# Kernel tuning notes

Measured on AMD Instinct MI355X. Metric: run time of the kernel, lower is better.

## Reference

```python
import jax, jax.numpy as jnp
import numpy as np

N_NODES = 100000


def sage_conv(x, edge_index, W_l, b_l, W_r):
    # PyG SAGEConv (mean aggr): out = lin_l(mean_j x_j) + lin_r(x_i)
    src = edge_index[0]
    dst = edge_index[1]
    msg_sum = jax.ops.segment_sum(x[src], dst, num_segments=N_NODES)  # [N, d]
    deg = jax.ops.segment_sum(jnp.ones(src.shape[0], dtype=x.dtype), dst,
                              num_segments=N_NODES)  # [N]
    mean = msg_sum / jnp.maximum(deg, 1.0)[:, None]
    return mean @ W_l + b_l + x @ W_r


def setup_inputs() -> dict:
    key = jax.random.key(0)
    ks = jax.random.split(key, 8)
    d_in, hidden, d_out = 128, 256, 128
    n_edges = 1600000
    x = jax.random.normal(ks[0], (N_NODES, d_in), dtype=jnp.float32)
    edge_index = jax.random.randint(ks[1], (2, n_edges), 0, N_NODES, dtype=jnp.int64)
    s1 = 1.0 / np.sqrt(d_in)
    s2 = 1.0 / np.sqrt(hidden)
    return {
        "x": x,
        "edge_index": edge_index,
        "W_l1": jax.random.uniform(ks[2], (d_in, hidden), jnp.float32, -s1, s1),
        "b_l1": jnp.zeros((hidden,), jnp.float32),
        "W_r1": jax.random.uniform(ks[3], (d_in, hidden), jnp.float32, -s1, s1),
        "W_l2": jax.random.uniform(ks[4], (hidden, d_out), jnp.float32, -s2, s2),
        "b_l2": jnp.zeros((d_out,), jnp.float32),
        "W_r2": jax.random.uniform(ks[5], (hidden, d_out), jnp.float32, -s2, s2),
    }


def reference(x, edge_index, W_l1, b_l1, W_r1, W_l2, b_l2, W_r2):
    h = jax.nn.relu(sage_conv(x, edge_index, W_l1, b_l1, W_r1))
    return sage_conv(h, edge_index, W_l2, b_l2, W_r2)
```

## Files before the change

kernel.cpp:

```cpp
#include <hip/hip_runtime.h>

#define N_NODES 100000
#define NPAD 100096
#define NBLK 391

using bf16x8 = __attribute__((ext_vector_type(8))) short;
using f32x4  = __attribute__((ext_vector_type(4))) float;

__device__ inline short f2bf(float f) {
    unsigned int u = __float_as_uint(f);
    unsigned int r = (u + 0x7FFFu + ((u >> 16) & 1u)) >> 16;
    return (short)r;
}
__device__ inline float bf2f_lo(unsigned int w) { return __uint_as_float(w << 16); }
__device__ inline float bf2f_hi(unsigned int w) { return __uint_as_float(w & 0xFFFF0000u); }

__device__ inline bool xcd_map(int bid, int& row, int& col) {
    const int RP = (NBLK + 7) / 8;
    const int xcd = bid & 7;
    const int i = bid >> 3;
    row = xcd * RP + (i >> 1);
    col = i & 1;
    return row < NBLK;
}
#define GEMM_GRID (8 * 2 * ((NBLK + 7) / 8))

__global__ __launch_bounds__(256)
void cbuck_kernel(const int* __restrict__ dst, int* __restrict__ bucket_cnt, int E) {
    __shared__ int cnt[NBLK];
    const int tid = threadIdx.x;
    for (int i = tid; i < NBLK; i += 256) cnt[i] = 0;
    __syncthreads();
    const int e0 = blockIdx.x * 4096;
    #pragma unroll
    for (int k = 0; k < 16; ++k) {
        int e = e0 + k * 256 + tid;
        if (e < E) atomicAdd(&cnt[dst[e] >> 8], 1);
    }
    __syncthreads();
    for (int i = tid; i < NBLK; i += 256)
        if (cnt[i]) atomicAdd(&bucket_cnt[i], cnt[i]);
}

__global__ void scan391_kernel(const int* __restrict__ bucket_cnt, int* __restrict__ bucket_base,
                               int* __restrict__ bucket_cursor, int* __restrict__ offsets) {
    __shared__ int s[512];
    int t = threadIdx.x;
    int v = (t < NBLK) ? bucket_cnt[t] : 0;
    s[t] = v;
    __syncthreads();
    #pragma unroll
    for (int off = 1; off < 512; off <<= 1) {
        int u = (t >= off) ? s[t - off] : 0;
        __syncthreads();
        s[t] += u;
        __syncthreads();
    }
    if (t < NBLK) {
        int excl = s[t] - v;
        bucket_base[t] = excl;
        bucket_cursor[t] = excl;
    }
    if (t == NBLK - 1) {
        bucket_base[NBLK] = s[t];
        offsets[N_NODES] = s[t];
    }
}

__global__ __launch_bounds__(256)
void bin_kernel(const int* __restrict__ src, const int* __restrict__ dst,
                int* __restrict__ bucket_cursor, unsigned int* __restrict__ bin, int E) {
    __shared__ int cnt[NBLK];
    __shared__ int base_l[NBLK];
    const int tid = threadIdx.x;
    const int e0 = blockIdx.x * 4096;
    for (int i = tid; i < NBLK; i += 256) cnt[i] = 0;
    __syncthreads();
    int myb[16]; unsigned myv[16];
    #pragma unroll
    for (int k = 0; k < 16; ++k) {
        int e = e0 + k * 256 + tid;
        if (e < E) {
            int d = dst[e];
            myb[k] = d >> 8;
            myv[k] = (unsigned)src[e] | ((unsigned)(d & 255) << 20);
            atomicAdd(&cnt[myb[k]], 1);
        } else myb[k] = -1;
    }
    __syncthreads();
    for (int i = tid; i < NBLK; i += 256) {
        int c = cnt[i];
        base_l[i] = c ? atomicAdd(&bucket_cursor[i], c) : 0;
        cnt[i] = 0;
    }
    __syncthreads();
    #pragma unroll
    for (int k = 0; k < 16; ++k) {
        if (myb[k] >= 0) {
            int slot = base_l[myb[k]] + atomicAdd(&cnt[myb[k]], 1);
            bin[slot] = myv[k];
        }
    }
}

__global__ __launch_bounds__(256)
void place_kernel(const unsigned int* __restrict__ bin, const int* __restrict__ bucket_base,
                  int* __restrict__ offsets, int* __restrict__ sorted) {
    __shared__ int cnt[256];
    __shared__ int cur[256];
    __shared__ int wsum[4];
    const int b = blockIdx.x, tid = threadIdx.x;
    const int lane = tid & 63, wave = tid >> 6;
    const int s = bucket_base[b];
    const int e = bucket_base[b + 1];
    cnt[tid] = 0;
    __syncthreads();
    for (int i = s + tid; i < e; i += 256) atomicAdd(&cnt[bin[i] >> 20], 1);
    __syncthreads();
    int v = cnt[tid];
    int x = v;
    #pragma unroll
    for (int off = 1; off < 64; off <<= 1) {
        int t = __shfl_up(x, off, 64);
        if (lane >= off) x += t;
    }
    if (lane == 63) wsum[wave] = x;
    __syncthreads();
    int woff = 0;
    #pragma unroll
    for (int w = 0; w < 4; ++w) if (w < wave) woff += wsum[w];
    int excl = s + woff + x - v;
    cur[tid] = excl;
    int node = b * 256 + tid;
    if (node < N_NODES) offsets[node] = excl;
    __syncthreads();
    for (int i = s + tid; i < e; i += 256) {
        unsigned w = bin[i];
        int p = atomicAdd(&cur[w >> 20], 1);
        sorted[p] = (int)(w & 0xFFFFFu);
    }
}

__global__ __launch_bounds__(256)
void prep_kernel(const float* __restrict__ x, short* __restrict__ xrow, short* __restrict__ xpack,
                 const float* __restrict__ Wl1, const float* __restrict__ Wr1,
                 const float* __restrict__ Wl2, const float* __restrict__ Wr2,
                 short* __restrict__ wl1p, short* __restrict__ wr1p,
                 short* __restrict__ wl2p, short* __restrict__ wr2p) {
    int t = blockIdx.x * 256 + threadIdx.x;
    if (t < N_NODES * 16) {
        int row = t >> 4;
        int kc = (t & 15) << 3;
        const float4 v0 = *(const float4*)(x + (size_t)row * 128 + kc);
        const float4 v1 = *(const float4*)(x + (size_t)row * 128 + kc + 4);
        __align__(16) short s[8] = {f2bf(v0.x), f2bf(v0.y), f2bf(v0.z), f2bf(v0.w),
                                    f2bf(v1.x), f2bf(v1.y), f2bf(v1.z), f2bf(v1.w)};
        *(int4*)(xrow + (size_t)row * 128 + kc) = *(const int4*)s;
        size_t pidx = ((size_t)(row >> 4) * 16 + (kc >> 3)) * 128 + (size_t)(row & 15) * 8;
        *(int4*)(xpack + pidx) = *(const int4*)s;
        return;
    }
    int u = t - N_NODES * 16;
    if (u >= 4 * 32768) return;
    const int w = u >> 15;
    const int t2 = u & 32767;
    const float* W; short* P; int K, NC;
    if (w == 0)      { W = Wl1; P = wl1p; K = 128; NC = 256; }
    else if (w == 1) { W = Wr1; P = wr1p; K = 128; NC = 256; }
    else if (w == 2) { W = Wl2; P = wl2p; K = 256; NC = 128; }
    else             { W = Wr2; P = wr2p; K = 256; NC = 128; }
    int k = t2 / NC, c = t2 % NC;
    P[((size_t)(c >> 4) * (K >> 3) + (k >> 3)) * 128 + (size_t)(c & 15) * 8 + (k & 7)] = f2bf(W[t2]);
}

template<int MODE>
__global__ __launch_bounds__(512)
void aggregate128_kernel(const short* __restrict__ feat, const int* __restrict__ offsets,
                         const int* __restrict__ srcs,
                         short* __restrict__ outpack, float* __restrict__ outf) {
    int node = blockIdx.x * 8 + (threadIdx.x >> 6);
    if (node >= N_NODES) return;
    const int lane = threadIdx.x & 63;
    const int g = lane >> 4, p = lane & 15;
    const int s = offsets[node], e = offsets[node + 1];
    const float inv = 1.0f / (float)max(e - s, 1);
    float acc[8] = {0.f, 0.f, 0.f, 0.f, 0.f, 0.f, 0.f, 0.f};
    for (int j = s + g; j < e; j += 8) {
        const int j2 = j + 4;
        const bool h2 = (j2 < e);
        const int i0 = srcs[j];
        const int i1 = h2 ? srcs[j2] : i0;
        const uint4 w0 = *(const uint4*)(feat + (size_t)i0 * 128 + p * 8);
        const uint4 w1 = *(const uint4*)(feat + (size_t)i1 * 128 + p * 8);
        acc[0] += bf2f_lo(w0.x); acc[1] += bf2f_hi(w0.x);
        acc[2] += bf2f_lo(w0.y); acc[3] += bf2f_hi(w0.y);
        acc[4] += bf2f_lo(w0.z); acc[5] += bf2f_hi(w0.z);
        acc[6] += bf2f_lo(w0.w); acc[7] += bf2f_hi(w0.w);
        if (h2) {
            acc[0] += bf2f_lo(w1.x); acc[1] += bf2f_hi(w1.x);
            acc[2] += bf2f_lo(w1.y); acc[3] += bf2f_hi(w1.y);
            acc[4] += bf2f_lo(w1.z); acc[5] += bf2f_hi(w1.z);
            acc[6] += bf2f_lo(w1.w); acc[7] += bf2f_hi(w1.w);
        }
    }
    #pragma unroll
    for (int t = 0; t < 8; ++t) acc[t] += __shfl_xor(acc[t], 16, 64);
    #pragma unroll
    for (int t = 0; t < 8; ++t) acc[t] += __shfl_xor(acc[t], 32, 64);
    if (g != 0) return;
    if (MODE == 0) {
        __align__(16) short r[8];
        #pragma unroll
        for (int t = 0; t < 8; ++t) r[t] = f2bf(acc[t] * inv);
        size_t pidx = ((size_t)(node >> 4) * 16 + p) * 128 + (size_t)(node & 15) * 8;
        *(int4*)(outpack + pidx) = *(const int4*)r;
    } else {
        float* o = outf + (size_t)node * 128 + p * 8;
        float4 q0 = *(const float4*)o;
        float4 q1 = *(const float4*)(o + 4);
        q0.x += acc[0] * inv; q0.y += acc[1] * inv; q0.z += acc[2] * inv; q0.w += acc[3] * inv;
        q1.x += acc[4] * inv; q1.y += acc[5] * inv; q1.z += acc[6] * inv; q1.w += acc[7] * inv;
        *(float4*)o = q0;
        *(float4*)(o + 4) = q1;
    }
}

__global__ __launch_bounds__(256)
void gemm1_kernel(const short* __restrict__ A0, const short* __restrict__ A1,
                  const short* __restrict__ B0, const short* __restrict__ B1,
                  const float* __restrict__ bias, short* __restrict__ opack) {
    constexpr int KB = 16, KS = 4, S = 8;
    __shared__ float sC[4][32][132];
    int rowBlk, colHalf;
    if (!xcd_map(blockIdx.x, rowBlk, colHalf)) return;
    const int tid = threadIdx.x, wave = tid >> 6, lane = tid & 63;
    const int lhi = lane >> 4, llo = lane & 15;
    const int rowBase = rowBlk * 256 + wave * 64;
    const int colBase = colHalf * 128;
    const int rowTile = rowBase >> 4, colTile = colBase >> 4;

    f32x4 acc[4][8];
    #pragma unroll
    for (int i = 0; i < 4; ++i)
        #pragma unroll
        for (int j = 0; j < 8; ++j)
            #pragma unroll
            for (int r = 0; r < 4; ++r) acc[i][j][r] = 0.f;

    bf16x8 a[4];
    #pragma unroll
    for (int i = 0; i < 4; ++i)
        a[i] = *(const bf16x8*)(A0 + ((size_t)(rowTile + i) * KB + lhi) * 128 + (size_t)llo * 8);

    #pragma unroll
    for (int s = 0; s < S; ++s) {
        const short* B = (s >= KS) ? B1 : B0;
        const int kb = (s - (s >= KS ? KS : 0)) * 4 + lhi;
        bf16x8 b[8];
        #pragma unroll
        for (int j = 0; j < 8; ++j)
            b[j] = *(const bf16x8*)(B + ((size_t)(colTile + j) * KB + kb) * 128 + (size_t)llo * 8);
        bf16x8 an[4];
        if (s + 1 < S) {
            const int s1 = s + 1;
            const short* A = (s1 >= KS) ? A1 : A0;
            const int kb1 = (s1 - (s1 >= KS ? KS : 0)) * 4 + lhi;
            #pragma unroll
            for (int i = 0; i < 4; ++i)
                an[i] = *(const bf16x8*)(A + ((size_t)(rowTile + i) * KB + kb1) * 128 + (size_t)llo * 8);
        }
        #pragma unroll
        for (int i = 0; i < 4; ++i)
            #pragma unroll
            for (int j = 0; j < 8; ++j)
                acc[i][j] = __builtin_amdgcn_mfma_f32_16x16x32_bf16(a[i], b[j], acc[i][j], 0, 0, 0);
        if (s + 1 < S) {
            #pragma unroll
            for (int i = 0; i < 4; ++i) a[i] = an[i];
        }
    }

    #pragma unroll
    for (int j = 0; j < 8; ++j) {
        float bv = bias[colBase + j * 16 + llo];
        #pragma unroll
        for (int i = 0; i < 4; ++i)
            #pragma unroll
            for (int r = 0; r < 4; ++r)
                acc[i][j][r] = fmaxf(acc[i][j][r] + bv, 0.f);
    }

    #pragma unroll
    for (int half = 0; half < 2; ++half) {
        #pragma unroll
        for (int i2 = 0; i2 < 2; ++i2) {
            const int i = half * 2 + i2;
            #pragma unroll
            for (int j = 0; j < 8; ++j)
                #pragma unroll
                for (int r = 0; r < 4; ++r)
                    sC[wave][i2 * 16 + lhi * 4 + r][j * 16 + llo] = acc[i][j][r];
        }
        #pragma unroll
        for (int it = 0; it < 8; ++it) {
            const int r = it * 4 + (lane >> 4);
            const int c = (lane & 15) * 8;
            const int grow = rowBase + half * 32 + r;
            if (grow < N_NODES) {
                float4 v0 = *(const float4*)&sC[wave][r][c];
                float4 v1 = *(const float4*)&sC[wave][r][c + 4];
                __align__(16) short sv[8] = {f2bf(v0.x), f2bf(v0.y), f2bf(v0.z), f2bf(v0.w),
                                             f2bf(v1.x), f2bf(v1.y), f2bf(v1.z), f2bf(v1.w)};
                size_t pidx = ((size_t)(grow >> 4) * 32 + ((colBase + c) >> 3)) * 128
                            + (size_t)(grow & 15) * 8;
                *(int4*)(opack + pidx) = *(const int4*)sv;
            }
        }
    }
}

__global__ __launch_bounds__(256)
void gemm2_kernel(const short* __restrict__ A, const short* __restrict__ B0,
                  const short* __restrict__ B1, const float* __restrict__ bias,
                  short* __restrict__ prow, float* __restrict__ qf32) {
    constexpr int KB = 32, S = 8;
    __shared__ float sC[4][32][68];
    int rowBlk, colHalf;
    if (!xcd_map(blockIdx.x, rowBlk, colHalf)) return;
    const int tid = threadIdx.x, wave = tid >> 6, lane = tid & 63;
    const int lhi = lane >> 4, llo = lane & 15;
    const int rowBase = rowBlk * 256 + wave * 64;
    const int colBase = colHalf * 64;
    const int rowTile = rowBase >> 4, colTile = colBase >> 4;

    f32x4 accp[4][4], accq[4][4];
    #pragma unroll
    for (int i = 0; i < 4; ++i)
        #pragma unroll
        for (int j = 0; j < 4; ++j)
            #pragma unroll
            for (int r = 0; r < 4; ++r) { accp[i][j][r] = 0.f; accq[i][j][r] = 0.f; }

    bf16x8 a[4];
    #pragma unroll
    for (int i = 0; i < 4; ++i)
        a[i] = *(const bf16x8*)(A + ((size_t)(rowTile + i) * KB + lhi) * 128 + (size_t)llo * 8);

    #pragma unroll
    for (int s = 0; s < S; ++s) {
        const int kb = s * 4 + lhi;
        bf16x8 b0[4], b1[4];
        #pragma unroll
        for (int j = 0; j < 4; ++j) {
            b0[j] = *(const bf16x8*)(B0 + ((size_t)(colTile + j) * KB + kb) * 128 + (size_t)llo * 8);
            b1[j] = *(const bf16x8*)(B1 + ((size_t)(colTile + j) * KB + kb) * 128 + (size_t)llo * 8);
        }
        bf16x8 an[4];
        if (s + 1 < S) {
            const int kb1 = (s + 1) * 4 + lhi;
            #pragma unroll
            for (int i = 0; i < 4; ++i)
                an[i] = *(const bf16x8*)(A + ((size_t)(rowTile + i) * KB + kb1) * 128 + (size_t)llo * 8);
        }
        #pragma unroll
        for (int i = 0; i < 4; ++i)
            #pragma unroll
            for (int j = 0; j < 4; ++j) {
                accp[i][j] = __builtin_amdgcn_mfma_f32_16x16x32_bf16(a[i], b0[j], accp[i][j], 0, 0, 0);
                accq[i][j] = __builtin_amdgcn_mfma_f32_16x16x32_bf16(a[i], b1[j], accq[i][j], 0, 0, 0);
            }
        if (s + 1 < S) {
            #pragma unroll
            for (int i = 0; i < 4; ++i) a[i] = an[i];
        }
    }

    #pragma unroll
    for (int half = 0; half < 2; ++half) {
        #pragma unroll
        for (int i2 = 0; i2 < 2; ++i2) {
            const int i = half * 2 + i2;
            #pragma unroll
            for (int j = 0; j < 4; ++j)
                #pragma unroll
                for (int r = 0; r < 4; ++r)
                    sC[wave][i2 * 16 + lhi * 4 + r][j * 16 + llo] = accp[i][j][r];
        }
        #pragma unroll
        for (int it = 0; it < 4; ++it) {
            const int r = it * 8 + (lane >> 3);
            const int c = (lane & 7) * 8;
            const int grow = rowBase + half * 32 + r;
            if (grow < N_NODES) {
                float4 v0 = *(const float4*)&sC[wave][r][c];
                float4 v1 = *(const float4*)&sC[wave][r][c + 4];
                __align__(16) short sv[8] = {f2bf(v0.x), f2bf(v0.y), f2bf(v0.z), f2bf(v0.w),
                                             f2bf(v1.x), f2bf(v1.y), f2bf(v1.z), f2bf(v1.w)};
                *(int4*)(prow + (size_t)grow * 128 + colBase + c) = *(const int4*)sv;
            }
        }
    }

    #pragma unroll
    for (int j = 0; j < 4; ++j) {
        float bv = bias[colBase + j * 16 + llo];
        #pragma unroll
        for (int i = 0; i < 4; ++i)
            #pragma unroll
            for (int r = 0; r < 4; ++r) accq[i][j][r] += bv;
    }
    #pragma unroll
    for (int half = 0; half < 2; ++half) {
        #pragma unroll
        for (int i2 = 0; i2 < 2; ++i2) {
            const int i = half * 2 + i2;
            #pragma unroll
            for (int j = 0; j < 4; ++j)
                #pragma unroll
                for (int r = 0; r < 4; ++r)
                    sC[wave][i2 * 16 + lhi * 4 + r][j * 16 + llo] = accq[i][j][r];
        }
        #pragma unroll
        for (int it = 0; it < 4; ++it) {
            const int r = it * 8 + (lane >> 3);
            const int c = (lane & 7) * 8;
            const int grow = rowBase + half * 32 + r;
            if (grow < N_NODES) {
                float4 v0 = *(const float4*)&sC[wave][r][c];
                float4 v1 = *(const float4*)&sC[wave][r][c + 4];
                *(float4*)(qf32 + (size_t)grow * 128 + colBase + c) = v0;
                *(float4*)(qf32 + (size_t)grow * 128 + colBase + c + 4) = v1;
            }
        }
    }
}

extern "C" void kernel_launch(void* const* d_in, const int* in_sizes, int n_in,
                              void* d_out, int out_size, void* d_ws, size_t ws_size,
                              hipStream_t stream) {
    const float* x   = (const float*)d_in[0];
    const int*   ei  = (const int*)d_in[1];
    const float* Wl1 = (const float*)d_in[2];
    const float* b1  = (const float*)d_in[3];
    const float* Wr1 = (const float*)d_in[4];
    const float* Wl2 = (const float*)d_in[5];
    const float* b2  = (const float*)d_in[6];
    const float* Wr2 = (const float*)d_in[7];
    const int E = in_sizes[1] / 2;
    const int* src = ei;
    const int* dst = ei + E;

    short* h_pack = (short*)d_ws;
    short* agg1p  = h_pack + (size_t)NPAD * 256;
    short* x_row  = agg1p  + (size_t)NPAD * 128;
    short* x_pack = x_row  + (size_t)NPAD * 128;
    short* p_row  = x_pack + (size_t)NPAD * 128;
    short* wl1p   = p_row  + (size_t)NPAD * 128;
    short* wr1p   = wl1p + 32768;
    short* wl2p   = wr1p + 32768;
    short* wr2p   = wl2p + 32768;
    int* bucket_cnt    = (int*)(wr2p + 32768);
    int* bucket_base   = bucket_cnt + NBLK + 1;
    int* bucket_cursor = bucket_base + NBLK + 1;
    int* offsets       = bucket_cursor + NBLK + 1;
    unsigned int* bin  = (unsigned int*)(offsets + N_NODES + 1);
    int* sorted        = (int*)(bin + E);

    const int nbin = (E + 4095) / 4096;

    hipMemsetAsync(bucket_cnt, 0, (NBLK + 1) * sizeof(int), stream);
    cbuck_kernel<<<nbin, 256, 0, stream>>>(dst, bucket_cnt, E);
    scan391_kernel<<<1, 512, 0, stream>>>(bucket_cnt, bucket_base, bucket_cursor, offsets);
    bin_kernel<<<nbin, 256, 0, stream>>>(src, dst, bucket_cursor, bin, E);
    place_kernel<<<NBLK, 256, 0, stream>>>(bin, bucket_base, offsets, sorted);

    prep_kernel<<<(N_NODES * 16 + 4 * 32768 + 255) / 256, 256, 0, stream>>>(
        x, x_row, x_pack, Wl1, Wr1, Wl2, Wr2, wl1p, wr1p, wl2p, wr2p);

    aggregate128_kernel<0><<<(N_NODES + 7) / 8, 512, 0, stream>>>(x_row, offsets, sorted, agg1p, nullptr);
    gemm1_kernel<<<GEMM_GRID, 256, 0, stream>>>(agg1p, x_pack, wl1p, wr1p, b1, h_pack);

    gemm2_kernel<<<GEMM_GRID, 256, 0, stream>>>(h_pack, wl2p, wr2p, b2, p_row, (float*)d_out);
    aggregate128_kernel<1><<<(N_NODES + 7) / 8, 512, 0, stream>>>(p_row, offsets, sorted, nullptr, (float*)d_out);
}
```

Measured before the change: 299.0 us.

## Slice gather feature tables by column so each XCD gathers from L2

Stores the bf16 feature tables (x and the layer-2 projection) as 8 column slices of 16 features each, one contiguous slice table per slice. The new aggregation kernel maps blockIdx&7 to a slice, so each XCD gathers only from its own table of about 3.2 MB, which can stay resident in L2 instead of scattering random reads over the full 25 MB table. The trade-off is that edge indices are re-read 8 times, each gather is only 32 bytes, and many lanes sit idle when a node has fewer than 32 neighbours.

```diff
diff --git a/kernel.cpp b/kernel.cpp
--- a/kernel.cpp
+++ b/kernel.cpp
@@ -142,7 +142,7 @@
 }
 
 __global__ __launch_bounds__(256)
-void prep_kernel(const float* __restrict__ x, short* __restrict__ xrow, short* __restrict__ xpack,
+void prep_kernel(const float* __restrict__ x, short* __restrict__ xslice, short* __restrict__ xpack,
                  const float* __restrict__ Wl1, const float* __restrict__ Wr1,
                  const float* __restrict__ Wl2, const float* __restrict__ Wr2,
                  short* __restrict__ wl1p, short* __restrict__ wr1p,
@@ -155,7 +155,8 @@
         const float4 v1 = *(const float4*)(x + (size_t)row * 128 + kc + 4);
         __align__(16) short s[8] = {f2bf(v0.x), f2bf(v0.y), f2bf(v0.z), f2bf(v0.w),
                                     f2bf(v1.x), f2bf(v1.y), f2bf(v1.z), f2bf(v1.w)};
-        *(int4*)(xrow + (size_t)row * 128 + kc) = *(const int4*)s;
+        size_t sidx = ((size_t)(kc >> 4) * NPAD + row) * 16 + (kc & 8);
+        *(int4*)(xslice + sidx) = *(const int4*)s;
         size_t pidx = ((size_t)(row >> 4) * 16 + (kc >> 3)) * 128 + (size_t)(row & 15) * 8;
         *(int4*)(xpack + pidx) = *(const int4*)s;
         return;
@@ -175,53 +176,54 @@
 
 template<int MODE>
 __global__ __launch_bounds__(512)
-void aggregate128_kernel(const short* __restrict__ feat, const int* __restrict__ offsets,
-                         const int* __restrict__ srcs,
-                         short* __restrict__ outpack, float* __restrict__ outf) {
-    int node = blockIdx.x * 8 + (threadIdx.x >> 6);
-    if (node >= N_NODES) return;
-    const int lane = threadIdx.x & 63;
-    const int g = lane >> 4, p = lane & 15;
-    const int s = offsets[node], e = offsets[node + 1];
-    const float inv = 1.0f / (float)max(e - s, 1);
-    float acc[8] = {0.f, 0.f, 0.f, 0.f, 0.f, 0.f, 0.f, 0.f};
-    for (int j = s + g; j < e; j += 8) {
-        const int j2 = j + 4;
-        const bool h2 = (j2 < e);
-        const int i0 = srcs[j];
-        const int i1 = h2 ? srcs[j2] : i0;
-        const uint4 w0 = *(const uint4*)(feat + (size_t)i0 * 128 + p * 8);
-        const uint4 w1 = *(const uint4*)(feat + (size_t)i1 * 128 + p * 8);
-        acc[0] += bf2f_lo(w0.x); acc[1] += bf2f_hi(w0.x);
-        acc[2] += bf2f_lo(w0.y); acc[3] += bf2f_hi(w0.y);
-        acc[4] += bf2f_lo(w0.z); acc[5] += bf2f_hi(w0.z);
-        acc[6] += bf2f_lo(w0.w); acc[7] += bf2f_hi(w0.w);
-        if (h2) {
-            acc[0] += bf2f_lo(w1.x); acc[1] += bf2f_hi(w1.x);
-            acc[2] += bf2f_lo(w1.y); acc[3] += bf2f_hi(w1.y);
-            acc[4] += bf2f_lo(w1.z); acc[5] += bf2f_hi(w1.z);
-            acc[6] += bf2f_lo(w1.w); acc[7] += bf2f_hi(w1.w);
-        }
-    }
-    #pragma unroll
-    for (int t = 0; t < 8; ++t) acc[t] += __shfl_xor(acc[t], 16, 64);
-    #pragma unroll
-    for (int t = 0; t < 8; ++t) acc[t] += __shfl_xor(acc[t], 32, 64);
-    if (g != 0) return;
-    if (MODE == 0) {
-        __align__(16) short r[8];
-        #pragma unroll
-        for (int t = 0; t < 8; ++t) r[t] = f2bf(acc[t] * inv);
-        size_t pidx = ((size_t)(node >> 4) * 16 + p) * 128 + (size_t)(node & 15) * 8;
-        *(int4*)(outpack + pidx) = *(const int4*)r;
-    } else {
-        float* o = outf + (size_t)node * 128 + p * 8;
-        float4 q0 = *(const float4*)o;
-        float4 q1 = *(const float4*)(o + 4);
-        q0.x += acc[0] * inv; q0.y += acc[1] * inv; q0.z += acc[2] * inv; q0.w += acc[3] * inv;
-        q1.x += acc[4] * inv; q1.y += acc[5] * inv; q1.z += acc[6] * inv; q1.w += acc[7] * inv;
-        *(float4*)o = q0;
-        *(float4*)(o + 4) = q1;
+void aggslice_kernel(const short* __restrict__ tab0, const int* __restrict__ offsets,
+                     const int* __restrict__ srcs,
+                     short* __restrict__ outpack, float* __restrict__ outf) {
+    const int slice = blockIdx.x & 7;
+    const int nbase = (blockIdx.x >> 3) * 32;
+    const int wave = threadIdx.x >> 6, lane = threadIdx.x & 63;
+    const int g = lane >> 1;
+    const int k = lane & 1;
+    const short* tab = tab0 + (size_t)slice * NPAD * 16;
+    #pragma unroll
+    for (int t = 0; t < 4; ++t) {
+        const int node = nbase + wave * 4 + t;
+        if (node >= N_NODES) return;
+        const int s = offsets[node], e = offsets[node + 1];
+        const float inv = 1.0f / (float)max(e - s, 1);
+        float acc[8] = {0.f, 0.f, 0.f, 0.f, 0.f, 0.f, 0.f, 0.f};
+        for (int j = s + g; j < e; j += 32) {
+            const int idx = srcs[j];
+            const uint4 w = *(const uint4*)(tab + (size_t)idx * 16 + k * 8);
+            acc[0] += bf2f_lo(w.x); acc[1] += bf2f_hi(w.x);
+            acc[2] += bf2f_lo(w.y); acc[3] += bf2f_hi(w.y);
+            acc[4] += bf2f_lo(w.z); acc[5] += bf2f_hi(w.z);
+            acc[6] += bf2f_lo(w.w); acc[7] += bf2f_hi(w.w);
+        }
+        #pragma unroll
+        for (int off = 2; off <= 32; off <<= 1)
+            #pragma unroll
+            for (int q = 0; q < 8; ++q) acc[q] += __shfl_xor(acc[q], off, 64);
+        if (g == 0) {
+            if (MODE == 0) {
+                __align__(16) short r[8];
+                #pragma unroll
+                for (int q = 0; q < 8; ++q) r[q] = f2bf(acc[q] * inv);
+                size_t pidx = ((size_t)(node >> 4) * 16 + 2 * slice + k) * 128
+                            + (size_t)(node & 15) * 8;
+                *(int4*)(outpack + pidx) = *(const int4*)r;
+            } else {
+                float* o = outf + (size_t)node * 128 + slice * 16 + k * 8;
+                float4 q0 = *(const float4*)o;
+                float4 q1 = *(const float4*)(o + 4);
+                q0.x += acc[0] * inv; q0.y += acc[1] * inv;
+                q0.z += acc[2] * inv; q0.w += acc[3] * inv;
+                q1.x += acc[4] * inv; q1.y += acc[5] * inv;
+                q1.z += acc[6] * inv; q1.w += acc[7] * inv;
+                *(float4*)o = q0;
+                *(float4*)(o + 4) = q1;
+            }
+        }
     }
 }
 
@@ -322,7 +324,7 @@
 __global__ __launch_bounds__(256)
 void gemm2_kernel(const short* __restrict__ A, const short* __restrict__ B0,
                   const short* __restrict__ B1, const float* __restrict__ bias,
-                  short* __restrict__ prow, float* __restrict__ qf32) {
+                  short* __restrict__ pslice, float* __restrict__ qf32) {
     constexpr int KB = 32, S = 8;
     __shared__ float sC[4][32][68];
     int rowBlk, colHalf;
@@ -396,7 +398,9 @@
                 float4 v1 = *(const float4*)&sC[wave][r][c + 4];
                 __align__(16) short sv[8] = {f2bf(v0.x), f2bf(v0.y), f2bf(v0.z), f2bf(v0.w),
                                              f2bf(v1.x), f2bf(v1.y), f2bf(v1.z), f2bf(v1.w)};
-                *(int4*)(prow + (size_t)grow * 128 + colBase + c) = *(const int4*)sv;
+                const int cc = colBase + c;
+                size_t sidx = ((size_t)(cc >> 4) * NPAD + grow) * 16 + (cc & 8);
+                *(int4*)(pslice + sidx) = *(const int4*)sv;
             }
         }
     }
@@ -450,15 +454,15 @@
     const int* src = ei;
     const int* dst = ei + E;
 
-    short* h_pack = (short*)d_ws;
-    short* agg1p  = h_pack + (size_t)NPAD * 256;
-    short* x_row  = agg1p  + (size_t)NPAD * 128;
-    short* x_pack = x_row  + (size_t)NPAD * 128;
-    short* p_row  = x_pack + (size_t)NPAD * 128;
-    short* wl1p   = p_row  + (size_t)NPAD * 128;
-    short* wr1p   = wl1p + 32768;
-    short* wl2p   = wr1p + 32768;
-    short* wr2p   = wl2p + 32768;
+    short* h_pack  = (short*)d_ws;
+    short* agg1p   = h_pack  + (size_t)NPAD * 256;
+    short* x_slice = agg1p   + (size_t)NPAD * 128;
+    short* x_pack  = x_slice + (size_t)NPAD * 128;
+    short* p_slice = x_pack  + (size_t)NPAD * 128;
+    short* wl1p    = p_slice + (size_t)NPAD * 128;
+    short* wr1p    = wl1p + 32768;
+    short* wl2p    = wr1p + 32768;
+    short* wr2p    = wl2p + 32768;
     int* bucket_cnt    = (int*)(wr2p + 32768);
     int* bucket_base   = bucket_cnt + NBLK + 1;
     int* bucket_cursor = bucket_base + NBLK + 1;
@@ -467,6 +471,7 @@
     int* sorted        = (int*)(bin + E);
 
     const int nbin = (E + 4095) / 4096;
+    const int agg_grid = 8 * ((N_NODES + 31) / 32);
 
     hipMemsetAsync(bucket_cnt, 0, (NBLK + 1) * sizeof(int), stream);
     cbuck_kernel<<<nbin, 256, 0, stream>>>(dst, bucket_cnt, E);
@@ -475,11 +480,11 @@
     place_kernel<<<NBLK, 256, 0, stream>>>(bin, bucket_base, offsets, sorted);
 
     prep_kernel<<<(N_NODES * 16 + 4 * 32768 + 255) / 256, 256, 0, stream>>>(
-        x, x_row, x_pack, Wl1, Wr1, Wl2, Wr2, wl1p, wr1p, wl2p, wr2p);
-
-    aggregate128_kernel<0><<<(N_NODES + 7) / 8, 512, 0, stream>>>(x_row, offsets, sorted, agg1p, nullptr);
+        x, x_slice, x_pack, Wl1, Wr1, Wl2, Wr2, wl1p, wr1p, wl2p, wr2p);
+
+    aggslice_kernel<0><<<agg_grid, 512, 0, stream>>>(x_slice, offsets, sorted, agg1p, nullptr);
     gemm1_kernel<<<GEMM_GRID, 256, 0, stream>>>(agg1p, x_pack, wl1p, wr1p, b1, h_pack);
 
-    gemm2_kernel<<<GEMM_GRID, 256, 0, stream>>>(h_pack, wl2p, wr2p, b2, p_row, (float*)d_out);
-    aggregate128_kernel<1><<<(N_NODES + 7) / 8, 512, 0, stream>>>(p_row, offsets, sorted, nullptr, (float*)d_out);
-}
+    gemm2_kernel<<<GEMM_GRID, 256, 0, stream>>>(h_pack, wl2p, wr2p, b2, p_slice, (float*)d_out);
+    aggslice_kernel<1><<<agg_grid, 512, 0, stream>>>(p_slice, offsets, sorted, nullptr, (float*)d_out);
+}
```

New measurement: 813.0 us. +171.9%, slower.
